# Kernel optimization log

Hardware: AMD Instinct MI355X
Metric: run time of the kernel (lower is better)

Reference implementation:

```python
import jax, jax.numpy as jnp
import numpy as np

EPS = 1e-6

def _rmsnorm(x, g):
    return x * jax.lax.rsqrt(jnp.mean(x * x, axis=-1, keepdims=True) + EPS) * g

def _linear(x, w, b):
    # torch nn.Linear convention: w is [out, in]
    return jnp.einsum('bld,hd->blh', x, w) + b

def setup_inputs() -> dict:
    key = jax.random.key(0)
    ks = jax.random.split(key, 10)
    B, L, D, H = 4, 4096, 1024, 2048
    s = 0.02
    return {
        'x': jax.random.normal(ks[0], (B, L, D), jnp.float32),
        'hidden': jax.random.normal(ks[1], (B, H), jnp.float32),
        'w_forget': jax.random.normal(ks[2], (H, D), jnp.float32) * s,
        'b_forget': jnp.zeros((H,), jnp.float32),
        'w_input': jax.random.normal(ks[3], (H, D), jnp.float32) * s,
        'b_input': jnp.zeros((H,), jnp.float32),
        'w_hout': jax.random.normal(ks[4], (D, H), jnp.float32) * s,
        'b_hout': jnp.zeros((D,), jnp.float32),
        'w_fc': jax.random.normal(ks[5], (H, D), jnp.float32) * s,
        'b_fc': jnp.zeros((H,), jnp.float32),
        'w_fc_act': jax.random.normal(ks[6], (H, D), jnp.float32) * s,
        'b_fc_act': jnp.zeros((H,), jnp.float32),
        'w_fout': jax.random.normal(ks[7], (D, H), jnp.float32) * s,
        'b_fout': jnp.zeros((D,), jnp.float32),
        'g_norm1': jnp.ones((D,), jnp.float32),
        'g_norm2': jnp.ones((D,), jnp.float32),
    }

def reference(x, hidden, w_forget, b_forget, w_input, b_input, w_hout, b_hout,
              w_fc, b_fc, w_fc_act, b_fc_act, w_fout, b_fout, g_norm1, g_norm2):
    H = hidden.shape[-1]
    # --- QGRU sub-block (pre-norm residual) ---
    xr = x
    xn = _rmsnorm(x, g_norm1)
    decay = jnp.linspace(0.0, 1.0, H, dtype=x.dtype)  # [H]
    remember = jax.nn.sigmoid(_linear(xn, w_forget, b_forget)) * decay  # [B,L,H]
    forget = 1.0 - remember
    inp = jnp.tanh(_linear(xn, w_input, b_input))
    # inclusive linear recurrence h[t] = forget[t]*h[t-1] + remember[t]*inp[t]
    def combine(c1, c2):
        a1, b1 = c1
        a2, b2 = c2
        return (a2 * a1, a2 * b1 + b2)
    _, h_inner = jax.lax.associative_scan(combine, (forget, inp * remember), axis=1)
    # fold in initial hidden state: h = h_inner + hidden * cumprod(forget)
    h = h_inner + hidden[:, None, :] * jnp.cumprod(forget, axis=1)  # [B,L,H]
    y = jnp.einsum('blh,dh->bld', h, w_hout) + b_hout
    x1 = y + xr  # dropout is identity in eval
    # --- FFN SwiGLU sub-block (pre-norm residual) ---
    xn2 = _rmsnorm(x1, g_norm2)
    ff = _linear(xn2, w_fc, b_fc) * jax.nn.silu(_linear(xn2, w_fc_act, b_fc_act))
    out = jnp.einsum('blh,dh->bld', ff, w_fout) + b_fout + x1
    return (out, h[:, -1, :])
```

## Files before the change

kernel.cpp:

```cpp
#include <hip/hip_runtime.h>
#include <hip/hip_bf16.h>

typedef __bf16 bf16x8 __attribute__((ext_vector_type(8)));
typedef __bf16 bf16x4 __attribute__((ext_vector_type(4)));
typedef float floatx4 __attribute__((ext_vector_type(4)));

#define LFULL 4096

__device__ __forceinline__ void gll16(const __bf16* g, __bf16* l) {
    __builtin_amdgcn_global_load_lds(
        (const __attribute__((address_space(1))) void*)g,
        (__attribute__((address_space(3))) void*)l, 16, 0, 0);
}

template <int RD>
__global__ __launch_bounds__(512, 2) void gemm_bt(
    const __bf16* __restrict__ A, const __bf16* __restrict__ Bw,
    const float* __restrict__ bias, const void* __restrict__ Rp,
    void* __restrict__ Cp, int K, int N, int sT, int t0)
{
    __shared__ __align__(16) __bf16 As[4][256][32];
    __shared__ __align__(16) __bf16 Bs[4][256][32];

    const int tid  = threadIdx.x;

    const int nwg = gridDim.x * gridDim.y;
    int bid = blockIdx.y * gridDim.x + blockIdx.x;
    bid = (bid & 7) * (nwg >> 3) + (bid >> 3);
    const int m0 = (bid / gridDim.x) * 256;
    const int n0 = (bid % gridDim.x) * 256;

    const int wave = tid >> 6;
    const int lane = tid & 63;
    const int wm   = (wave & 1) * 128;
    const int wn   = (wave >> 1) * 64;
    const int q    = lane >> 4;
    const int ml   = lane & 15;
    const int ks   = (q ^ ((ml >> 1) & 3)) * 8;

    const int t8 = tid * 8;
    const int rA = tid >> 2;
    const int cg = ((tid & 3) ^ ((tid >> 3) & 3)) * 8;
    const __bf16* gA1 = A  + (size_t)(m0 + rA) * K + cg;
    const __bf16* gA2 = A  + (size_t)(m0 + 128 + rA) * K + cg;
    const __bf16* gB1 = Bw + (size_t)(n0 + rA) * K + cg;
    const __bf16* gB2 = Bw + (size_t)(n0 + 128 + rA) * K + cg;

    floatx4 acc[8][4] = {};
    int sb = 0;

#define STAGE() do { \
        __bf16* la = (__bf16*)As[sb & 3]; \
        __bf16* lb = (__bf16*)Bs[sb & 3]; \
        gll16(gA1, la + t8); \
        gll16(gA2, la + 4096 + t8); \
        gll16(gB1, lb + t8); \
        gll16(gB2, lb + 4096 + t8); \
        gA1 += 32; gA2 += 32; gB1 += 32; gB2 += 32; ++sb; \
    } while (0)

#define COMPUTE(CB) do { \
        const __bf16* Ab = &As[CB][0][0]; \
        const __bf16* Bb = &Bs[CB][0][0]; \
        bf16x8 af[8], bfr[4]; \
        _Pragma("unroll") \
        for (int i = 0; i < 8; i++) \
            af[i] = *(const bf16x8*)(Ab + (wm + i * 16 + ml) * 32 + ks); \
        _Pragma("unroll") \
        for (int j = 0; j < 4; j++) \
            bfr[j] = *(const bf16x8*)(Bb + (wn + j * 16 + ml) * 32 + ks); \
        __builtin_amdgcn_s_setprio(1); \
        _Pragma("unroll") \
        for (int i = 0; i < 8; i++) \
            _Pragma("unroll") \
            for (int j = 0; j < 4; j++) \
                acc[i][j] = __builtin_amdgcn_mfma_f32_16x16x32_bf16(af[i], bfr[j], acc[i][j], 0, 0, 0); \
        __builtin_amdgcn_s_setprio(0); \
    } while (0)

    const int NT = K >> 5;
    STAGE(); STAGE(); STAGE();
    asm volatile("s_waitcnt vmcnt(8)" ::: "memory");
    __builtin_amdgcn_s_barrier();
    __builtin_amdgcn_sched_barrier(0);

    for (int kt = 0; kt < NT; ++kt) {
        if (kt + 3 < NT) STAGE();
        COMPUTE(kt & 3);
        const int rem = NT - 1 - kt;
        if (rem >= 3)      { asm volatile("s_waitcnt vmcnt(8)" ::: "memory"); }
        else if (rem == 2) { asm volatile("s_waitcnt vmcnt(4)" ::: "memory"); }
        else if (rem == 1) { asm volatile("s_waitcnt vmcnt(0)" ::: "memory"); }
        if (rem > 0) {
            __builtin_amdgcn_s_barrier();
            __builtin_amdgcn_sched_barrier(0);
        }
    }

#undef STAGE
#undef COMPUTE

    const int Tmask = (1 << sT) - 1;
#pragma unroll
    for (int i = 0; i < 8; i++) {
#pragma unroll
        for (int j = 0; j < 4; j++) {
            const int n = n0 + wn + j * 16 + ml;
            const float bv = bias[n];
            const float dec = (float)n * (1.0f / 2047.0f);
#pragma unroll
            for (int r = 0; r < 4; r++) {
                const int m = m0 + wm + i * 16 + q * 4 + r;
                float v = acc[i][j][r] + bv;
                if (RD == 1) {
                    const int gm = ((m >> sT) * LFULL) + t0 + (m & Tmask);
                    v += ((const float*)Rp)[(size_t)gm * N + n];
                    ((__bf16*)Cp)[(size_t)m * N + n] = (__bf16)v;
                } else if (RD == 2) {
                    v += (float)((const __bf16*)Rp)[(size_t)m * N + n];
                    const int gm = ((m >> sT) * LFULL) + t0 + (m & Tmask);
                    ((float*)Cp)[(size_t)gm * N + n] = v;
                } else if (RD == 3) {
                    const float sl = v / (1.f + __expf(-v));
                    const float z1 = (float)((const __bf16*)Rp)[(size_t)m * N + n];
                    ((__bf16*)Cp)[(size_t)m * N + n] = (__bf16)(z1 * sl);
                } else if (RD == 4) {
                    const float rr = dec / (1.f + __expf(-v));
                    ((__bf16*)Cp)[(size_t)m * N + n] = (__bf16)rr;
                } else if (RD == 5) {
                    const float e = __expf(2.f * v);
                    const float th = 1.f - 2.f / (e + 1.f);
                    ((__bf16*)Cp)[(size_t)m * N + n] = (__bf16)th;
                } else {
                    ((__bf16*)Cp)[(size_t)m * N + n] = (__bf16)v;
                }
            }
        }
    }
}

__global__ __launch_bounds__(256) void cvt_w(
    const float* __restrict__ s0, const float* __restrict__ s1,
    const float* __restrict__ s2, const float* __restrict__ s3,
    const float* __restrict__ s4, const float* __restrict__ s5,
    __bf16* __restrict__ dst)
{
    const float* srcs[6] = {s0, s1, s2, s3, s4, s5};
    const float* s = srcs[blockIdx.y];
    __bf16* d = dst + (size_t)blockIdx.y * 2097152;
    const int i = (blockIdx.x * 256 + threadIdx.x) * 8;
    float4 f0 = *(const float4*)(s + i);
    float4 f1 = *(const float4*)(s + i + 4);
    bf16x8 o;
    o[0] = (__bf16)f0.x; o[1] = (__bf16)f0.y; o[2] = (__bf16)f0.z; o[3] = (__bf16)f0.w;
    o[4] = (__bf16)f1.x; o[5] = (__bf16)f1.y; o[6] = (__bf16)f1.z; o[7] = (__bf16)f1.w;
    *(bf16x8*)(d + i) = o;
}

__global__ __launch_bounds__(256) void rmsnorm_f32in(
    const float* __restrict__ x, const float* __restrict__ g,
    __bf16* __restrict__ o, int sT, int t0)
{
    const int r = blockIdx.x;
    const int grow = ((r >> sT) * LFULL) + t0 + (r & ((1 << sT) - 1));
    const float* xr = x + (size_t)grow * 1024;
    const int tid = threadIdx.x;

    float4 v = *(const float4*)(xr + tid * 4);
    float vv[4] = {v.x, v.y, v.z, v.w};
    float ss = vv[0] * vv[0] + vv[1] * vv[1] + vv[2] * vv[2] + vv[3] * vv[3];
#pragma unroll
    for (int off = 32; off > 0; off >>= 1) ss += __shfl_down(ss, off);

    __shared__ float red[4];
    if ((tid & 63) == 0) red[tid >> 6] = ss;
    __syncthreads();
    const float tot = red[0] + red[1] + red[2] + red[3];
    const float scale = rsqrtf(tot * (1.0f / 1024.0f) + 1e-6f);

    float4 g4 = *(const float4*)(g + tid * 4);
    float gg[4] = {g4.x, g4.y, g4.z, g4.w};
    bf16x4 ov;
#pragma unroll
    for (int e = 0; e < 4; e++) ov[e] = (__bf16)(vv[e] * scale * gg[e]);
    *(bf16x4*)(o + (size_t)r * 1024 + tid * 4) = ov;
}

__global__ __launch_bounds__(256) void rmsnorm_b16in(
    const __bf16* __restrict__ x, const float* __restrict__ g,
    __bf16* __restrict__ o)
{
    const int r = blockIdx.x;
    const __bf16* xr = x + (size_t)r * 1024;
    const int tid = threadIdx.x;

    bf16x4 v = *(const bf16x4*)(xr + tid * 4);
    float vv[4];
#pragma unroll
    for (int e = 0; e < 4; e++) vv[e] = (float)v[e];
    float ss = vv[0] * vv[0] + vv[1] * vv[1] + vv[2] * vv[2] + vv[3] * vv[3];
#pragma unroll
    for (int off = 32; off > 0; off >>= 1) ss += __shfl_down(ss, off);

    __shared__ float red[4];
    if ((tid & 63) == 0) red[tid >> 6] = ss;
    __syncthreads();
    const float tot = red[0] + red[1] + red[2] + red[3];
    const float scale = rsqrtf(tot * (1.0f / 1024.0f) + 1e-6f);

    float4 g4 = *(const float4*)(g + tid * 4);
    float gg[4] = {g4.x, g4.y, g4.z, g4.w};
    bf16x4 ov;
#pragma unroll
    for (int e = 0; e < 4; e++) ov[e] = (__bf16)(vv[e] * scale * gg[e]);
    *(bf16x4*)(o + (size_t)r * 1024 + tid * 4) = ov;
}

__global__ __launch_bounds__(256) void scan_pass1(
    const __bf16* __restrict__ rr, const __bf16* __restrict__ th,
    float* __restrict__ Ach, float* __restrict__ Bch, int T)
{
    const int h0 = threadIdx.x * 8;
    const int s = blockIdx.x;
    const int b = blockIdx.y;
    const int NSC = T >> 5;
    size_t p = ((size_t)b * T + s * 32) * 2048 + h0;
    float Aa[8], Bv[8];
#pragma unroll
    for (int e = 0; e < 8; e++) { Aa[e] = 1.f; Bv[e] = 0.f; }
    for (int t = 0; t < 32; t++, p += 2048) {
        bf16x8 rv = *(const bf16x8*)(rr + p);
        bf16x8 tv = *(const bf16x8*)(th + p);
#pragma unroll
        for (int e = 0; e < 8; e++) {
            const float r = (float)rv[e];
            const float a = 1.f - r;
            Aa[e] *= a;
            Bv[e] = a * Bv[e] + r * (float)tv[e];
        }
    }
    const size_t qq = (size_t)(b * NSC + s) * 2048 + h0;
#pragma unroll
    for (int e = 0; e < 8; e++) { Ach[qq + e] = Aa[e]; Bch[qq + e] = Bv[e]; }
}

__global__ __launch_bounds__(256) void scan_pass2(
    const float* __restrict__ Ach, const float* __restrict__ Bch,
    float* __restrict__ hst, const float* __restrict__ hidden,
    float* __restrict__ state, float* __restrict__ hlast,
    int NSC, int first, int last)
{
    const int idx = blockIdx.x * 256 + threadIdx.x;
    const int b = idx >> 11;
    const int h = idx & 2047;
    float hs = first ? hidden[idx] : state[idx];
    size_t qq = (size_t)b * NSC * 2048 + h;
#pragma unroll 4
    for (int s = 0; s < NSC; s++, qq += 2048) {
        hst[qq] = hs;
        hs = Ach[qq] * hs + Bch[qq];
    }
    state[idx] = hs;
    if (last) hlast[idx] = hs;
}

__global__ __launch_bounds__(256) void scan_pass3(
    __bf16* __restrict__ rio, const __bf16* __restrict__ th,
    const float* __restrict__ hst, int T)
{
    const int h0 = threadIdx.x * 8;
    const int s = blockIdx.x;
    const int b = blockIdx.y;
    const int NSC = T >> 5;
    float hp[8];
    const size_t qq = (size_t)(b * NSC + s) * 2048 + h0;
#pragma unroll
    for (int e = 0; e < 8; e++) hp[e] = hst[qq + e];
    size_t p = ((size_t)b * T + s * 32) * 2048 + h0;
    for (int t = 0; t < 32; t++, p += 2048) {
        bf16x8 rv = *(const bf16x8*)(rio + p);
        bf16x8 tv = *(const bf16x8*)(th + p);
        bf16x8 ov;
#pragma unroll
        for (int e = 0; e < 8; e++) {
            const float r = (float)rv[e];
            hp[e] = (1.f - r) * hp[e] + r * (float)tv[e];
            ov[e] = (__bf16)hp[e];
        }
        *(bf16x8*)(rio + p) = ov;
    }
}

extern "C" void kernel_launch(void* const* d_in, const int* in_sizes, int n_in,
                              void* d_out, int out_size, void* d_ws, size_t ws_size,
                              hipStream_t stream)
{
    const float* x        = (const float*)d_in[0];
    const float* hidden   = (const float*)d_in[1];
    const float* w_forget = (const float*)d_in[2];
    const float* b_forget = (const float*)d_in[3];
    const float* w_input  = (const float*)d_in[4];
    const float* b_input  = (const float*)d_in[5];
    const float* w_hout   = (const float*)d_in[6];
    const float* b_hout   = (const float*)d_in[7];
    const float* w_fc     = (const float*)d_in[8];
    const float* b_fc     = (const float*)d_in[9];
    const float* w_fc_act = (const float*)d_in[10];
    const float* b_fc_act = (const float*)d_in[11];
    const float* w_fout   = (const float*)d_in[12];
    const float* b_fout   = (const float*)d_in[13];
    const float* g_norm1  = (const float*)d_in[14];
    const float* g_norm2  = (const float*)d_in[15];

    float* out   = (float*)d_out;
    float* hlast = out + (size_t)16384 * 1024;

    int T = 4096;
    for (;;) {
        size_t need = 25165824ull + (size_t)4 * T * 12288 + 3ull * 4 * (T / 32) * 2048 * 4 + 65536;
        if (need <= ws_size || T == 256) break;
        T >>= 1;
    }
    const int NC = 4096 / T;
    int sT = 0; while ((1 << sT) < T) sT++;
    const int Mc = 4 * T;
    const int NSC = T >> 5;

    char* p = (char*)d_ws;
    __bf16* wb = (__bf16*)p; p += 25165824ull;
    __bf16* xn = (__bf16*)p; p += (size_t)Mc * 1024 * 2;
    __bf16* zf = (__bf16*)p; p += (size_t)Mc * 2048 * 2;
    __bf16* zi = (__bf16*)p; p += (size_t)Mc * 2048 * 2;
    __bf16* x1 = (__bf16*)p; p += (size_t)Mc * 1024 * 2;
    float* Ach = (float*)p;  p += (size_t)4 * NSC * 2048 * 4;
    float* Bch = (float*)p;  p += (size_t)4 * NSC * 2048 * 4;
    float* hst = (float*)p;  p += (size_t)4 * NSC * 2048 * 4;
    float* state = (float*)p;

    __bf16* wb_f  = wb;
    __bf16* wb_i  = wb + 2097152;
    __bf16* wb_fc = wb + 2 * 2097152;
    __bf16* wb_fa = wb + 3 * 2097152;
    __bf16* wb_h  = wb + 4 * 2097152;
    __bf16* wb_o  = wb + 5 * 2097152;

    cvt_w<<<dim3(1024, 6), 256, 0, stream>>>(w_forget, w_input, w_fc, w_fc_act, w_hout, w_fout, wb);

    for (int c = 0; c < NC; c++) {
        const int t0 = c * T;
        rmsnorm_f32in<<<Mc, 256, 0, stream>>>(x, g_norm1, xn, sT, t0);
        gemm_bt<4><<<dim3(8, Mc / 256), 512, 0, stream>>>(xn, wb_f, b_forget, nullptr, zf, 1024, 2048, sT, t0);
        gemm_bt<5><<<dim3(8, Mc / 256), 512, 0, stream>>>(xn, wb_i, b_input,  nullptr, zi, 1024, 2048, sT, t0);
        scan_pass1<<<dim3(NSC, 4), 256, 0, stream>>>(zf, zi, Ach, Bch, T);
        scan_pass2<<<32, 256, 0, stream>>>(Ach, Bch, hst, hidden, state, hlast, NSC,
                                           (c == 0) ? 1 : 0, (c == NC - 1) ? 1 : 0);
        scan_pass3<<<dim3(NSC, 4), 256, 0, stream>>>(zf, zi, hst, T);
        gemm_bt<1><<<dim3(4, Mc / 256), 512, 0, stream>>>(zf, wb_h, b_hout, x, x1, 2048, 1024, sT, t0);
        rmsnorm_b16in<<<Mc, 256, 0, stream>>>(x1, g_norm2, xn);
        gemm_bt<0><<<dim3(8, Mc / 256), 512, 0, stream>>>(xn, wb_fc, b_fc,     nullptr, zf, 1024, 2048, sT, t0);
        gemm_bt<3><<<dim3(8, Mc / 256), 512, 0, stream>>>(xn, wb_fa, b_fc_act, zf, zf, 1024, 2048, sT, t0);
        gemm_bt<2><<<dim3(4, Mc / 256), 512, 0, stream>>>(zf, wb_o, b_fout, x1, out, 2048, 1024, sT, t0);
    }
}
```

Baseline: 842.0 us.

## Split GEMM k-step into two half-tile phases interleaving LDS loads and prefetch

Restructures the GEMM main loop so each k-tile is processed in two halves. Each half loads fragments from LDS, issues part of the next global-to-LDS prefetch (A, then B), and synchronises with barriers before running its MFMA batch. This is a ping-pong style schedule meant to overlap memory traffic with matrix work and cut fragment register pressure. It adds several barriers per iteration, which can cost time if the waves do not stay in lockstep.

```diff
diff --git a/kernel.cpp b/kernel.cpp
--- a/kernel.cpp
+++ b/kernel.cpp
@@ -49,7 +49,7 @@
     floatx4 acc[8][4] = {};
     int sb = 0;
 
-#define STAGE() do { \
+#define STAGE_FULL() do { \
         __bf16* la = (__bf16*)As[sb & 3]; \
         __bf16* lb = (__bf16*)Bs[sb & 3]; \
         gll16(gA1, la + t8); \
@@ -59,46 +59,75 @@
         gA1 += 32; gA2 += 32; gB1 += 32; gB2 += 32; ++sb; \
     } while (0)
 
-#define COMPUTE(CB) do { \
-        const __bf16* Ab = &As[CB][0][0]; \
-        const __bf16* Bb = &Bs[CB][0][0]; \
-        bf16x8 af[8], bfr[4]; \
-        _Pragma("unroll") \
-        for (int i = 0; i < 8; i++) \
-            af[i] = *(const bf16x8*)(Ab + (wm + i * 16 + ml) * 32 + ks); \
-        _Pragma("unroll") \
-        for (int j = 0; j < 4; j++) \
-            bfr[j] = *(const bf16x8*)(Bb + (wn + j * 16 + ml) * 32 + ks); \
-        __builtin_amdgcn_s_setprio(1); \
-        _Pragma("unroll") \
-        for (int i = 0; i < 8; i++) \
-            _Pragma("unroll") \
-            for (int j = 0; j < 4; j++) \
-                acc[i][j] = __builtin_amdgcn_mfma_f32_16x16x32_bf16(af[i], bfr[j], acc[i][j], 0, 0, 0); \
-        __builtin_amdgcn_s_setprio(0); \
+#define STAGE_A() do { \
+        __bf16* la = (__bf16*)As[sb & 3]; \
+        gll16(gA1, la + t8); \
+        gll16(gA2, la + 4096 + t8); \
+        gA1 += 32; gA2 += 32; \
     } while (0)
 
+#define STAGE_B() do { \
+        __bf16* lb = (__bf16*)Bs[sb & 3]; \
+        gll16(gB1, lb + t8); \
+        gll16(gB2, lb + 4096 + t8); \
+        gB1 += 32; gB2 += 32; ++sb; \
+    } while (0)
+
     const int NT = K >> 5;
-    STAGE(); STAGE(); STAGE();
+    STAGE_FULL(); STAGE_FULL(); STAGE_FULL();
     asm volatile("s_waitcnt vmcnt(8)" ::: "memory");
     __builtin_amdgcn_s_barrier();
-    __builtin_amdgcn_sched_barrier(0);
 
     for (int kt = 0; kt < NT; ++kt) {
-        if (kt + 3 < NT) STAGE();
-        COMPUTE(kt & 3);
+        const int CB = kt & 3;
+        const __bf16* Ab = &As[CB][0][0];
+        const __bf16* Bb = &Bs[CB][0][0];
+        bf16x8 af[4], bfr[4];
+        const bool pre = (kt + 3 < NT);
+
+#pragma unroll
+        for (int i = 0; i < 4; i++)
+            af[i] = *(const bf16x8*)(Ab + (wm + i * 16 + ml) * 32 + ks);
+#pragma unroll
+        for (int j = 0; j < 4; j++)
+            bfr[j] = *(const bf16x8*)(Bb + (wn + j * 16 + ml) * 32 + ks);
+        if (pre) STAGE_A();
+        __builtin_amdgcn_s_barrier();
+        asm volatile("s_waitcnt lgkmcnt(0)" ::: "memory");
+        __builtin_amdgcn_sched_barrier(0);
+        __builtin_amdgcn_s_setprio(1);
+#pragma unroll
+        for (int i = 0; i < 4; i++)
+#pragma unroll
+            for (int j = 0; j < 4; j++)
+                acc[i][j] = __builtin_amdgcn_mfma_f32_16x16x32_bf16(af[i], bfr[j], acc[i][j], 0, 0, 0);
+        __builtin_amdgcn_s_setprio(0);
+        __builtin_amdgcn_s_barrier();
+
+#pragma unroll
+        for (int i = 0; i < 4; i++)
+            af[i] = *(const bf16x8*)(Ab + (wm + 64 + i * 16 + ml) * 32 + ks);
+        if (pre) STAGE_B();
+        __builtin_amdgcn_s_barrier();
+        asm volatile("s_waitcnt lgkmcnt(0)" ::: "memory");
+        __builtin_amdgcn_sched_barrier(0);
+        __builtin_amdgcn_s_setprio(1);
+#pragma unroll
+        for (int i = 0; i < 4; i++)
+#pragma unroll
+            for (int j = 0; j < 4; j++)
+                acc[4 + i][j] = __builtin_amdgcn_mfma_f32_16x16x32_bf16(af[i], bfr[j], acc[4 + i][j], 0, 0, 0);
+        __builtin_amdgcn_s_setprio(0);
         const int rem = NT - 1 - kt;
         if (rem >= 3)      { asm volatile("s_waitcnt vmcnt(8)" ::: "memory"); }
         else if (rem == 2) { asm volatile("s_waitcnt vmcnt(4)" ::: "memory"); }
         else if (rem == 1) { asm volatile("s_waitcnt vmcnt(0)" ::: "memory"); }
-        if (rem > 0) {
-            __builtin_amdgcn_s_barrier();
-            __builtin_amdgcn_sched_barrier(0);
-        }
-    }
-
-#undef STAGE
-#undef COMPUTE
+        __builtin_amdgcn_s_barrier();
+    }
+
+#undef STAGE_FULL
+#undef STAGE_A
+#undef STAGE_B
 
     const int Tmask = (1 << sT) - 1;
 #pragma unroll
```

New measurement: 752.1 us. 10.7% less time.

## Software-pipeline LDS fragment loads with MFMA in bf16 GEMM main loop

Applied to the files above, without the earlier changes.

Each K-tile is split into two halves of rows. The second half's A fragments are loaded while the first half's MFMAs run. The next tile's A and B fragments are prefetched from LDS during the current tile's MFMAs. The vmcnt waits are tightened so that the next stage is resident before the barrier. This is meant to hide ds_read latency behind matrix math, at the cost of extra live fragment registers under a 512x2 launch bound, which risks spilling.

```diff
diff --git a/kernel.cpp b/kernel.cpp
--- a/kernel.cpp
+++ b/kernel.cpp
@@ -59,46 +59,66 @@
         gA1 += 32; gA2 += 32; gB1 += 32; gB2 += 32; ++sb; \
     } while (0)
 
-#define COMPUTE(CB) do { \
-        const __bf16* Ab = &As[CB][0][0]; \
-        const __bf16* Bb = &Bs[CB][0][0]; \
-        bf16x8 af[8], bfr[4]; \
-        _Pragma("unroll") \
-        for (int i = 0; i < 8; i++) \
-            af[i] = *(const bf16x8*)(Ab + (wm + i * 16 + ml) * 32 + ks); \
-        _Pragma("unroll") \
-        for (int j = 0; j < 4; j++) \
-            bfr[j] = *(const bf16x8*)(Bb + (wn + j * 16 + ml) * 32 + ks); \
-        __builtin_amdgcn_s_setprio(1); \
-        _Pragma("unroll") \
-        for (int i = 0; i < 8; i++) \
-            _Pragma("unroll") \
-            for (int j = 0; j < 4; j++) \
-                acc[i][j] = __builtin_amdgcn_mfma_f32_16x16x32_bf16(af[i], bfr[j], acc[i][j], 0, 0, 0); \
-        __builtin_amdgcn_s_setprio(0); \
-    } while (0)
-
     const int NT = K >> 5;
     STAGE(); STAGE(); STAGE();
-    asm volatile("s_waitcnt vmcnt(8)" ::: "memory");
+    asm volatile("s_waitcnt vmcnt(4)" ::: "memory");
     __builtin_amdgcn_s_barrier();
     __builtin_amdgcn_sched_barrier(0);
 
+    bf16x8 afH0[4], bfr[4], af1[4];
+#pragma unroll
+    for (int i = 0; i < 4; i++)
+        afH0[i] = *(const bf16x8*)(&As[0][0][0] + (wm + i * 16 + ml) * 32 + ks);
+#pragma unroll
+    for (int j = 0; j < 4; j++)
+        bfr[j] = *(const bf16x8*)(&Bs[0][0][0] + (wn + j * 16 + ml) * 32 + ks);
+
     for (int kt = 0; kt < NT; ++kt) {
+        const __bf16* Ab  = &As[kt & 3][0][0];
+        const __bf16* Abn = &As[(kt + 1) & 3][0][0];
+        const __bf16* Bbn = &Bs[(kt + 1) & 3][0][0];
+        const bool more = (kt + 1 < NT);
+
         if (kt + 3 < NT) STAGE();
-        COMPUTE(kt & 3);
-        const int rem = NT - 1 - kt;
-        if (rem >= 3)      { asm volatile("s_waitcnt vmcnt(8)" ::: "memory"); }
-        else if (rem == 2) { asm volatile("s_waitcnt vmcnt(4)" ::: "memory"); }
-        else if (rem == 1) { asm volatile("s_waitcnt vmcnt(0)" ::: "memory"); }
-        if (rem > 0) {
+
+#pragma unroll
+        for (int i = 0; i < 4; i++)
+            af1[i] = *(const bf16x8*)(Ab + (wm + 64 + i * 16 + ml) * 32 + ks);
+
+        __builtin_amdgcn_s_setprio(1);
+#pragma unroll
+        for (int j = 0; j < 4; j++)
+#pragma unroll
+            for (int i = 0; i < 4; i++)
+                acc[i][j] = __builtin_amdgcn_mfma_f32_16x16x32_bf16(afH0[i], bfr[j], acc[i][j], 0, 0, 0);
+        __builtin_amdgcn_s_setprio(0);
+
+        if (more) {
+#pragma unroll
+            for (int i = 0; i < 4; i++)
+                afH0[i] = *(const bf16x8*)(Abn + (wm + i * 16 + ml) * 32 + ks);
+        }
+
+        __builtin_amdgcn_s_setprio(1);
+#pragma unroll
+        for (int j = 0; j < 4; j++) {
+#pragma unroll
+            for (int i = 0; i < 4; i++)
+                acc[4 + i][j] = __builtin_amdgcn_mfma_f32_16x16x32_bf16(af1[i], bfr[j], acc[4 + i][j], 0, 0, 0);
+            if (more)
+                bfr[j] = *(const bf16x8*)(Bbn + (wn + j * 16 + ml) * 32 + ks);
+        }
+        __builtin_amdgcn_s_setprio(0);
+
+        if (more) {
+            if (kt + 3 < NT) { asm volatile("s_waitcnt vmcnt(4)" ::: "memory"); }
+            else             { asm volatile("s_waitcnt vmcnt(0)" ::: "memory"); }
             __builtin_amdgcn_s_barrier();
             __builtin_amdgcn_sched_barrier(0);
         }
     }
 
 #undef STAGE
-#undef COMPUTE
 
     const int Tmask = (1 << sT) - 1;
 #pragma unroll
```

New measurement: 844.1 us. About the same (+0.2%).

## Software-pipeline LDS fragment reads with MFMA clusters in GEMM main loop

Applied to the files above, without the earlier changes.

Restructures the GEMM k-loop into half-tile MFMA clusters, with double-buffered A/B register fragments. LDS reads for the next cluster are issued before the current cluster's MFMAs, so shared-memory latency overlaps tensor-core work. The change also drops the XCD-aware block-index swizzle and goes back to plain blockIdx tile mapping, which can change L2 locality across chiplets. It adds more barriers per k-step and assumes NT is even.

```diff
diff --git a/kernel.cpp b/kernel.cpp
--- a/kernel.cpp
+++ b/kernel.cpp
@@ -23,12 +23,8 @@
     __shared__ __align__(16) __bf16 Bs[4][256][32];
 
     const int tid  = threadIdx.x;
-
-    const int nwg = gridDim.x * gridDim.y;
-    int bid = blockIdx.y * gridDim.x + blockIdx.x;
-    bid = (bid & 7) * (nwg >> 3) + (bid >> 3);
-    const int m0 = (bid / gridDim.x) * 256;
-    const int n0 = (bid % gridDim.x) * 256;
+    const int m0 = blockIdx.y * 256;
+    const int n0 = blockIdx.x * 256;
 
     const int wave = tid >> 6;
     const int lane = tid & 63;
@@ -59,46 +55,92 @@
         gA1 += 32; gA2 += 32; gB1 += 32; gB2 += 32; ++sb; \
     } while (0)
 
-#define COMPUTE(CB) do { \
-        const __bf16* Ab = &As[CB][0][0]; \
-        const __bf16* Bb = &Bs[CB][0][0]; \
-        bf16x8 af[8], bfr[4]; \
-        _Pragma("unroll") \
-        for (int i = 0; i < 8; i++) \
-            af[i] = *(const bf16x8*)(Ab + (wm + i * 16 + ml) * 32 + ks); \
+#define VM_LADDER(T) do { \
+        if ((T) + 3 < NT)       { asm volatile("s_waitcnt vmcnt(8)" ::: "memory"); } \
+        else if ((T) + 3 == NT) { asm volatile("s_waitcnt vmcnt(4)" ::: "memory"); } \
+        else if ((T) + 2 == NT) { asm volatile("s_waitcnt vmcnt(0)" ::: "memory"); } \
+    } while (0)
+
+#define CLUSTER(R0, AF, BF) do { \
+        __builtin_amdgcn_s_setprio(1); \
         _Pragma("unroll") \
         for (int j = 0; j < 4; j++) \
-            bfr[j] = *(const bf16x8*)(Bb + (wn + j * 16 + ml) * 32 + ks); \
-        __builtin_amdgcn_s_setprio(1); \
+            _Pragma("unroll") \
+            for (int i = 0; i < 4; i++) \
+                acc[(R0) + i][j] = __builtin_amdgcn_mfma_f32_16x16x32_bf16(AF[i], BF[j], acc[(R0) + i][j], 0, 0, 0); \
+        __builtin_amdgcn_s_setprio(0); \
+    } while (0)
+
+#define READ_A(DST, BUF, ROFF) do { \
+        const __bf16* _p = &As[BUF][0][0]; \
         _Pragma("unroll") \
-        for (int i = 0; i < 8; i++) \
-            _Pragma("unroll") \
-            for (int j = 0; j < 4; j++) \
-                acc[i][j] = __builtin_amdgcn_mfma_f32_16x16x32_bf16(af[i], bfr[j], acc[i][j], 0, 0, 0); \
-        __builtin_amdgcn_s_setprio(0); \
+        for (int i = 0; i < 4; i++) \
+            DST[i] = *(const bf16x8*)(_p + (wm + (ROFF) + i * 16 + ml) * 32 + ks); \
+    } while (0)
+
+#define READ_B(DST, BUF) do { \
+        const __bf16* _p = &Bs[BUF][0][0]; \
+        _Pragma("unroll") \
+        for (int j = 0; j < 4; j++) \
+            DST[j] = *(const bf16x8*)(_p + (wn + j * 16 + ml) * 32 + ks); \
     } while (0)
 
     const int NT = K >> 5;
     STAGE(); STAGE(); STAGE();
     asm volatile("s_waitcnt vmcnt(8)" ::: "memory");
+    __builtin_amdgcn_sched_barrier(0);
     __builtin_amdgcn_s_barrier();
-    __builtin_amdgcn_sched_barrier(0);
-
-    for (int kt = 0; kt < NT; ++kt) {
-        if (kt + 3 < NT) STAGE();
-        COMPUTE(kt & 3);
-        const int rem = NT - 1 - kt;
-        if (rem >= 3)      { asm volatile("s_waitcnt vmcnt(8)" ::: "memory"); }
-        else if (rem == 2) { asm volatile("s_waitcnt vmcnt(4)" ::: "memory"); }
-        else if (rem == 1) { asm volatile("s_waitcnt vmcnt(0)" ::: "memory"); }
-        if (rem > 0) {
-            __builtin_amdgcn_s_barrier();
-            __builtin_amdgcn_sched_barrier(0);
+
+    bf16x8 afq0[4], afq1[4], bfE[4], bfO[4];
+    READ_A(afq0, 0, 0);
+    READ_B(bfE, 0);
+
+    for (int u = 0; u < (NT >> 1); ++u) {
+        const int tE = 2 * u, tO = 2 * u + 1;
+
+        if (tE + 3 < NT) STAGE();
+        READ_A(afq1, tE & 3, 64);
+        VM_LADDER(tE);
+        __builtin_amdgcn_sched_barrier(0);
+        __builtin_amdgcn_s_barrier();
+        asm volatile("s_waitcnt lgkmcnt(4)" ::: "memory");
+        __builtin_amdgcn_sched_barrier(0);
+        CLUSTER(0, afq0, bfE);
+
+        READ_A(afq0, tO & 3, 0);
+        READ_B(bfO, tO & 3);
+        __builtin_amdgcn_sched_barrier(0);
+        __builtin_amdgcn_s_barrier();
+        asm volatile("s_waitcnt lgkmcnt(8)" ::: "memory");
+        __builtin_amdgcn_sched_barrier(0);
+        CLUSTER(4, afq1, bfE);
+
+        if (tO + 3 < NT) STAGE();
+        READ_A(afq1, tO & 3, 64);
+        VM_LADDER(tO);
+        __builtin_amdgcn_sched_barrier(0);
+        __builtin_amdgcn_s_barrier();
+        asm volatile("s_waitcnt lgkmcnt(4)" ::: "memory");
+        __builtin_amdgcn_sched_barrier(0);
+        CLUSTER(0, afq0, bfO);
+
+        if (tO + 1 < NT) {
+            READ_A(afq0, (tO + 1) & 3, 0);
+            READ_B(bfE, (tO + 1) & 3);
         }
+        __builtin_amdgcn_sched_barrier(0);
+        __builtin_amdgcn_s_barrier();
+        if (tO + 1 < NT) { asm volatile("s_waitcnt lgkmcnt(8)" ::: "memory"); }
+        else             { asm volatile("s_waitcnt lgkmcnt(0)" ::: "memory"); }
+        __builtin_amdgcn_sched_barrier(0);
+        CLUSTER(4, afq1, bfO);
     }
 
 #undef STAGE
-#undef COMPUTE
+#undef VM_LADDER
+#undef CLUSTER
+#undef READ_A
+#undef READ_B
 
     const int Tmask = (1 << sT) - 1;
 #pragma unroll
```

Measured after the change: 839.8 us. About the same (-0.3%).
